# Kernel tuning notes

Hardware: AMD Instinct MI355X
Metric: run time of the kernel (lower is better)

Reference implementation:

```python
import jax, jax.numpy as jnp
import numpy as np

EMBED_DIM = 1024
NUM_HEADS = 16
HEAD_DIM = EMBED_DIM // NUM_HEADS


def setup_inputs() -> dict:
    key = jax.random.key(0)
    ks = jax.random.split(key, 11)
    B, S, D = 4, 2048, EMBED_DIM
    s = 1.0 / np.sqrt(D)
    return {
        "q": jax.random.normal(ks[0], (B, S, D), jnp.float32),
        "k": jax.random.normal(ks[1], (B, S, D), jnp.float32),
        "v": jax.random.normal(ks[2], (B, S, D), jnp.float32),
        "Wq": jax.random.normal(ks[3], (D, D), jnp.float32) * s,
        "bq": jnp.zeros((D,), jnp.float32),
        "Wk": jax.random.normal(ks[4], (D, D), jnp.float32) * s,
        "bk": jnp.zeros((D,), jnp.float32),
        "Wv": jax.random.normal(ks[5], (D, D), jnp.float32) * s,
        "bv": jnp.zeros((D,), jnp.float32),
        "Wo": jax.random.normal(ks[6], (D, D), jnp.float32) * s,
        "bo": jnp.zeros((D,), jnp.float32),
    }


def reference(q, k, v, Wq, bq, Wk, bk, Wv, bv, Wo, bo):
    B, S, D = q.shape
    H, Hd = NUM_HEADS, HEAD_DIM
    # projections, split heads -> [B, H, S, Hd]
    qh = (q @ Wq + bq).reshape(B, S, H, Hd).transpose(0, 2, 1, 3)
    kh = (k @ Wk + bk).reshape(B, S, H, Hd).transpose(0, 2, 1, 3)
    vh = (v @ Wv + bv).reshape(B, S, H, Hd).transpose(0, 2, 1, 3)
    scale = 1.0 / jnp.sqrt(jnp.asarray(Hd, qh.dtype))
    scores = jnp.einsum('bhqd,bhkd->bhqk', qh, kh) * scale  # [B,H,S,S]
    attn = jax.nn.softmax(scores, axis=-1)  # dropout = identity in eval
    out = jnp.einsum('bhqk,bhkd->bhqd', attn, vh)
    out = out.transpose(0, 2, 1, 3).reshape(B, S, D)
    return out @ Wo + bo
```

## Files before the change

### kernel.cpp

```cpp
#include <hip/hip_runtime.h>

typedef __attribute__((ext_vector_type(8))) __bf16 bf16x8;
typedef __attribute__((ext_vector_type(4))) __bf16 bf16x4;
typedef __attribute__((ext_vector_type(4))) float f32x4;
typedef __attribute__((ext_vector_type(16))) float f32x16;
typedef __attribute__((ext_vector_type(4))) unsigned int u32x4;

#define GLDS(g, l) __builtin_amdgcn_global_load_lds( \
    (const __attribute__((address_space(1))) void*)(g), \
    (__attribute__((address_space(3))) void*)(l), 16, 0, 0)

__device__ __forceinline__ unsigned cvtpk_bf16(float lo, float hi) {
    unsigned r;
    asm("v_cvt_pk_bf16_f32 %0, %1, %2" : "=v"(r) : "v"(lo), "v"(hi));
    return r;
}
__device__ __forceinline__ void pl32swap(unsigned& a, unsigned& b) {
    asm("v_permlane32_swap_b32 %0, %1" : "+v"(a), "+v"(b));
}

__global__ __launch_bounds__(256) void cvt_tile(const float* __restrict__ q,
                                                const float* __restrict__ k,
                                                const float* __restrict__ v,
                                                __bf16* __restrict__ qo,
                                                __bf16* __restrict__ ko,
                                                __bf16* __restrict__ vo) {
    const float* src = blockIdx.z == 0 ? q : blockIdx.z == 1 ? k : v;
    __bf16* dst = blockIdx.z == 0 ? qo : blockIdx.z == 1 ? ko : vo;
    __shared__ __align__(16) __bf16 sb[128 * 64];
    const int t = threadIdx.x;
    const int m0 = blockIdx.x * 128, kk0 = blockIdx.y * 64;
    #pragma unroll
    for (int i = 0; i < 4; i++) {
        int cid = i * 256 + t;
        int r = cid >> 3, cc = cid & 7;
        const float* p = src + (size_t)(m0 + r) * 1024 + kk0 + cc * 8;
        float4 a = *(const float4*)p;
        float4 b2 = *(const float4*)(p + 4);
        bf16x8 o;
        o[0] = (__bf16)a.x;  o[1] = (__bf16)a.y;  o[2] = (__bf16)a.z;  o[3] = (__bf16)a.w;
        o[4] = (__bf16)b2.x; o[5] = (__bf16)b2.y; o[6] = (__bf16)b2.z; o[7] = (__bf16)b2.w;
        *(bf16x8*)((char*)sb + r * 128 + ((cc ^ (r & 7)) << 4)) = o;
    }
    __syncthreads();
    #pragma unroll
    for (int i = 0; i < 4; i++) {
        int cid = i * 256 + t;
        int ch = cid >> 7, r = cid & 127;
        bf16x8 o = *(const bf16x8*)((const char*)sb + r * 128 + ((ch ^ (r & 7)) << 4));
        size_t off = (((size_t)blockIdx.x * 32 + blockIdx.y * 2 + (ch >> 2)) * 4 + (ch & 3)) * 1024
                   + (size_t)r * 8;
        *(bf16x8*)(dst + off) = o;
    }
}

__global__ __launch_bounds__(256) void wtrans2(const float* __restrict__ W0,
                                               const float* __restrict__ W1,
                                               const float* __restrict__ W2,
                                               const float* __restrict__ W3,
                                               __bf16* __restrict__ O0,
                                               __bf16* __restrict__ O1,
                                               __bf16* __restrict__ O2,
                                               __bf16* __restrict__ O3) {
    const int z = blockIdx.z;
    const float* W = z == 0 ? W0 : z == 1 ? W1 : z == 2 ? W2 : W3;
    __bf16* Wt2 = z == 0 ? O0 : z == 1 ? O1 : z == 2 ? O2 : O3;
    __shared__ float lw[64][65];
    const int kt = blockIdx.y * 64, nt = blockIdx.x * 64;
    const int t = threadIdx.x;
    const int r = t >> 4;
    const int c4 = (t & 15) * 4;
    #pragma unroll
    for (int rr = 0; rr < 64; rr += 16) {
        float4 vv = *(const float4*)&W[(size_t)(kt + r + rr) * 1024 + nt + c4];
        lw[r + rr][c4 + 0] = vv.x; lw[r + rr][c4 + 1] = vv.y;
        lw[r + rr][c4 + 2] = vv.z; lw[r + rr][c4 + 3] = vv.w;
    }
    __syncthreads();
    #pragma unroll
    for (int rr = 0; rr < 64; rr += 16) {
        int n = nt + r + rr;
        bf16x4 ov;
        #pragma unroll
        for (int i = 0; i < 4; i++) ov[i] = (__bf16)lw[c4 + i][r + rr];
        int kg = kt + c4;
        size_t off = (((size_t)(n >> 7) * 32 + (kg >> 5)) * 4 + ((kg & 31) >> 3)) * 1024
                   + (size_t)(n & 127) * 8 + (kg & 7);
        *(bf16x4*)&Wt2[off] = ov;
    }
}

__global__ __launch_bounds__(256, 2)
void gemm_tt(const __bf16* __restrict__ A0, const __bf16* __restrict__ A1,
             const __bf16* __restrict__ A2,
             const __bf16* __restrict__ B0, const __bf16* __restrict__ B1,
             const __bf16* __restrict__ B2,
             const float* __restrict__ bi0, const float* __restrict__ bi1,
             const float* __restrict__ bi2,
             void* __restrict__ C0, void* __restrict__ C1, void* __restrict__ C2,
             int mode0) {
    __shared__ __align__(16) __bf16 sA[3 * 4096];
    __shared__ __align__(16) __bf16 sB[3 * 4096];
    const int y = blockIdx.y;
    const __bf16* At  = y == 0 ? A0 : y == 1 ? A1 : A2;
    const __bf16* Bt2 = y == 0 ? B0 : y == 1 ? B1 : B2;
    const float* bias = y == 0 ? bi0 : y == 1 ? bi1 : bi2;
    void* Cout        = y == 0 ? C0 : y == 1 ? C1 : C2;
    const int mode    = y == 0 ? mode0 : y + 1;

    const int t = threadIdx.x, l = t & 63, w = t >> 6;
    const int wr = w >> 1, wc = w & 1;
    const int bid = blockIdx.x, slot = bid >> 3;
    const int ytile = (bid & 7) * 8 + (slot & 7);
    const int xtile = slot >> 3;
    const __bf16* Ab = At + (size_t)ytile * 131072;
    const __bf16* Bb = Bt2 + (size_t)xtile * 131072;

#define GISSUE(ks_, buf_) do { \
    GLDS(Ab + (ks_) * 4096 + t * 8,        (char*)sA + (buf_) * 8192 + t * 16); \
    GLDS(Ab + (ks_) * 4096 + 2048 + t * 8, (char*)sA + (buf_) * 8192 + 4096 + t * 16); \
    GLDS(Bb + (ks_) * 4096 + t * 8,        (char*)sB + (buf_) * 8192 + t * 16); \
    GLDS(Bb + (ks_) * 4096 + 2048 + t * 8, (char*)sB + (buf_) * 8192 + 4096 + t * 16); \
} while (0)

    f32x4 acc[4][4];
    #pragma unroll
    for (int i = 0; i < 4; i++)
        #pragma unroll
        for (int j = 0; j < 4; j++) acc[i][j] = (f32x4){0.f, 0.f, 0.f, 0.f};

    GISSUE(0, 0);
    GISSUE(1, 1);
    int cur = 0;
    #pragma unroll 1
    for (int ks = 0; ks < 32; ++ks) {
        if (ks < 31) asm volatile("s_waitcnt vmcnt(4)" ::: "memory");
        else         asm volatile("s_waitcnt vmcnt(0)" ::: "memory");
        __builtin_amdgcn_s_barrier();
        __builtin_amdgcn_sched_barrier(0);
        if (ks + 2 < 32) GISSUE(ks + 2, cur >= 1 ? cur - 1 : 2);
        const __bf16* bA = sA + cur * 4096;
        const __bf16* bB = sB + cur * 4096;
        bf16x8 af[4], bfr[4];
        #pragma unroll
        for (int i = 0; i < 4; i++)
            af[i] = *(const bf16x8*)(bA + (l >> 4) * 1024 + (wr * 64 + i * 16 + (l & 15)) * 8);
        #pragma unroll
        for (int j = 0; j < 4; j++)
            bfr[j] = *(const bf16x8*)(bB + (l >> 4) * 1024 + (wc * 64 + j * 16 + (l & 15)) * 8);
        __builtin_amdgcn_s_setprio(1);
        #pragma unroll
        for (int i = 0; i < 4; i++)
            #pragma unroll
            for (int j = 0; j < 4; j++)
                acc[i][j] = __builtin_amdgcn_mfma_f32_16x16x32_bf16(af[i], bfr[j], acc[i][j], 0, 0, 0);
        __builtin_amdgcn_s_setprio(0);
        cur = cur == 2 ? 0 : cur + 1;
    }
#undef GISSUE

    const int m0 = ytile * 128, n0 = xtile * 128;
    #pragma unroll
    for (int j = 0; j < 4; j++) {
        int col = n0 + wc * 64 + j * 16 + (l & 15);
        float bv = bias[col];
        #pragma unroll
        for (int i = 0; i < 4; i++) {
            #pragma unroll
            for (int r = 0; r < 4; r++) {
                int row = m0 + wr * 64 + i * 16 + (l >> 4) * 4 + r;
                float vvv = acc[i][j][r] + bv;
                if (mode == 0) {
                    ((float*)Cout)[(size_t)row * 1024 + col] = vvv;
                } else if (mode == 1) {
                    ((__bf16*)Cout)[(size_t)row * 1024 + col] = (__bf16)(vvv * 0.18033688f);
                } else if (mode == 2) {
                    int b_ = row >> 11, s_ = row & 2047, h_ = col >> 6, hd_ = col & 63;
                    size_t off = ((size_t)(b_ * 16 + h_) * 32 + (s_ >> 6)) * 4096
                               + (size_t)(hd_ >> 3) * 512 + (s_ & 63) * 8 + (hd_ & 7);
                    ((__bf16*)Cout)[off] = (__bf16)vvv;
                } else {
                    int b_ = row >> 11, s_ = row & 2047, h_ = col >> 6, d_ = col & 63;
                    size_t off = ((size_t)(b_ * 16 + h_) * 32 + (s_ >> 6)) * 4096
                               + (size_t)((s_ & 63) >> 3) * 512 + (size_t)d_ * 8 + (s_ & 7);
                    ((__bf16*)Cout)[off] = (__bf16)vvv;
                }
            }
        }
    }
}

__global__ __launch_bounds__(256, 2)
void attn_fwd(const __bf16* __restrict__ Qp, const __bf16* __restrict__ Kt,
              const __bf16* __restrict__ Vtt, __bf16* __restrict__ AOt) {
    constexpr int S = 2048, D = 1024;
    __shared__ __align__(16) __bf16 sK[3 * 4096];
    __shared__ __align__(16) __bf16 sV[3 * 4096];
    const int t = threadIdx.x, l = t & 63, w = t >> 6;
    const int c = l & 31, g = l >> 5;
    const int bid = blockIdx.x, slot = bid >> 3;
    const int bh = (slot >> 3) * 8 + (bid & 7);
    const int qb = slot & 7;
    const int b = bh >> 4, h = bh & 15;
    const int q0 = qb * 256;
    const __bf16* Kb = Kt + (size_t)bh * 131072;
    const __bf16* Vb = Vtt + (size_t)bh * 131072;

    bf16x8 qf[2][4];
    #pragma unroll
    for (int qh = 0; qh < 2; qh++) {
        const __bf16* qp = Qp + (size_t)(b * S + q0 + w * 64 + qh * 32 + c) * D + h * 64;
        #pragma unroll
        for (int ks = 0; ks < 4; ks++)
            qf[qh][ks] = *(const bf16x8*)(qp + ks * 16 + g * 8);
    }
    const __bf16 one = (__bf16)1.0f;
    const bf16x8 ones = {one, one, one, one, one, one, one, one};
    asm volatile("s_waitcnt vmcnt(0)" ::: "memory");

#define AISSUE(ti_, buf_) do { \
    GLDS(Kb + (ti_) * 4096 + t * 8,        (char*)sK + (buf_) * 8192 + t * 16); \
    GLDS(Kb + (ti_) * 4096 + 2048 + t * 8, (char*)sK + (buf_) * 8192 + 4096 + t * 16); \
    GLDS(Vb + (ti_) * 4096 + t * 8,        (char*)sV + (buf_) * 8192 + t * 16); \
    GLDS(Vb + (ti_) * 4096 + 2048 + t * 8, (char*)sV + (buf_) * 8192 + 4096 + t * 16); \
} while (0)

    f32x16 acc[2][2];
    acc[0][0] = (f32x16){}; acc[0][1] = (f32x16){};
    acc[1][0] = (f32x16){}; acc[1][1] = (f32x16){};
    f32x16 accl[2];
    accl[0] = (f32x16){}; accl[1] = (f32x16){};

    AISSUE(0, 0);
    AISSUE(1, 1);
    int cur = 0;
    #pragma unroll 1
    for (int tile = 0; tile < 32; ++tile) {
        if (tile < 31) asm volatile("s_waitcnt vmcnt(4)" ::: "memory");
        else           asm volatile("s_waitcnt vmcnt(0)" ::: "memory");
        __builtin_amdgcn_s_barrier();
        __builtin_amdgcn_sched_barrier(0);
        if (tile + 2 < 32) AISSUE(tile + 2, cur >= 1 ? cur - 1 : 2);
        const __bf16* bK = sK + cur * 4096;
        const __bf16* bV = sV + cur * 4096;
        #pragma unroll
        for (int kt = 0; kt < 2; kt++) {
            bf16x8 kf[4];
            #pragma unroll
            for (int ks = 0; ks < 4; ks++)
                kf[ks] = *(const bf16x8*)(bK + ((2 * ks + g) * 64 + kt * 32 + c) * 8);
            bf16x8 vq0[2], vq1[2];
            #pragma unroll
            for (int ti = 0; ti < 2; ti++) {
                vq0[ti] = *(const bf16x8*)(bV + ((4 * kt + g) * 64 + ti * 32 + c) * 8);
                vq1[ti] = *(const bf16x8*)(bV + ((4 * kt + 2 + g) * 64 + ti * 32 + c) * 8);
            }
            #pragma unroll
            for (int qh = 0; qh < 2; qh++) {
                f32x16 St = {};
                __builtin_amdgcn_s_setprio(1);
                St = __builtin_amdgcn_mfma_f32_32x32x16_bf16(kf[0], qf[qh][0], St, 0, 0, 0);
                St = __builtin_amdgcn_mfma_f32_32x32x16_bf16(kf[1], qf[qh][1], St, 0, 0, 0);
                St = __builtin_amdgcn_mfma_f32_32x32x16_bf16(kf[2], qf[qh][2], St, 0, 0, 0);
                St = __builtin_amdgcn_mfma_f32_32x32x16_bf16(kf[3], qf[qh][3], St, 0, 0, 0);
                __builtin_amdgcn_s_setprio(0);
                #pragma unroll
                for (int r2 = 0; r2 < 16; r2++)
                    St[r2] = __builtin_amdgcn_exp2f(St[r2]);
                unsigned w0 = cvtpk_bf16(St[0], St[1]),   w1 = cvtpk_bf16(St[2], St[3]);
                unsigned w2 = cvtpk_bf16(St[4], St[5]),   w3 = cvtpk_bf16(St[6], St[7]);
                unsigned w4 = cvtpk_bf16(St[8], St[9]),   w5 = cvtpk_bf16(St[10], St[11]);
                unsigned w6 = cvtpk_bf16(St[12], St[13]), w7 = cvtpk_bf16(St[14], St[15]);
                pl32swap(w0, w2); pl32swap(w1, w3);
                pl32swap(w4, w6); pl32swap(w5, w7);
                bf16x8 pa0 = __builtin_bit_cast(bf16x8, (u32x4){w0, w1, w2, w3});
                bf16x8 pa1 = __builtin_bit_cast(bf16x8, (u32x4){w4, w5, w6, w7});
                __builtin_amdgcn_s_setprio(1);
                acc[qh][0] = __builtin_amdgcn_mfma_f32_32x32x16_bf16(pa0, vq0[0], acc[qh][0], 0, 0, 0);
                acc[qh][1] = __builtin_amdgcn_mfma_f32_32x32x16_bf16(pa0, vq0[1], acc[qh][1], 0, 0, 0);
                acc[qh][0] = __builtin_amdgcn_mfma_f32_32x32x16_bf16(pa1, vq1[0], acc[qh][0], 0, 0, 0);
                acc[qh][1] = __builtin_amdgcn_mfma_f32_32x32x16_bf16(pa1, vq1[1], acc[qh][1], 0, 0, 0);
                accl[qh] = __builtin_amdgcn_mfma_f32_32x32x16_bf16(pa0, ones, accl[qh], 0, 0, 0);
                accl[qh] = __builtin_amdgcn_mfma_f32_32x32x16_bf16(pa1, ones, accl[qh], 0, 0, 0);
                __builtin_amdgcn_s_setprio(0);
            }
        }
        cur = cur == 2 ? 0 : cur + 1;
    }
#undef AISSUE

    #pragma unroll
    for (int qh = 0; qh < 2; qh++)
        #pragma unroll
        for (int rq = 0; rq < 4; rq++)
            #pragma unroll
            for (int rr2 = 0; rr2 < 4; rr2++) {
                int reg = rq * 4 + rr2;
                int rloc = rr2 + 8 * rq + 4 * g;
                float rn = __builtin_amdgcn_rcpf(accl[qh][reg]);
                int qloc = w * 64 + qh * 32 + rloc;
                int mt = b * 16 + qb * 2 + (qloc >> 7);
                int mr = qloc & 127;
                size_t base = ((size_t)mt * 32 + h * 2) * 4096 + (size_t)(c >> 3) * 1024
                            + (size_t)mr * 8 + (c & 7);
                AOt[base] = (__bf16)(acc[qh][0][reg] * rn);
                AOt[base + 4096] = (__bf16)(acc[qh][1][reg] * rn);
            }
}

extern "C" void kernel_launch(void* const* d_in, const int* in_sizes, int n_in,
                              void* d_out, int out_size, void* d_ws, size_t ws_size,
                              hipStream_t stream) {
    const float* q  = (const float*)d_in[0];
    const float* k  = (const float*)d_in[1];
    const float* v  = (const float*)d_in[2];
    const float* Wq = (const float*)d_in[3];
    const float* bq = (const float*)d_in[4];
    const float* Wk = (const float*)d_in[5];
    const float* bk = (const float*)d_in[6];
    const float* Wv = (const float*)d_in[7];
    const float* bv = (const float*)d_in[8];
    const float* Wo = (const float*)d_in[9];
    const float* bo = (const float*)d_in[10];

    char* ws = (char*)d_ws;
    const size_t MiB = 1024 * 1024;
    __bf16* Atq = (__bf16*)(ws);
    __bf16* Atk = (__bf16*)(ws + 16 * MiB);
    __bf16* Atv = (__bf16*)(ws + 32 * MiB);
    __bf16* W2q = (__bf16*)(ws + 48 * MiB);
    __bf16* W2k = (__bf16*)(ws + 50 * MiB);
    __bf16* W2v = (__bf16*)(ws + 52 * MiB);
    __bf16* W2o = (__bf16*)(ws + 54 * MiB);
    __bf16* Qp  = (__bf16*)(ws + 56 * MiB);
    __bf16* Kt  = (__bf16*)(ws + 72 * MiB);
    __bf16* Vtt = (__bf16*)(ws + 88 * MiB);
    __bf16* AOt = (__bf16*)(ws);

    cvt_tile<<<dim3(64, 16, 3), 256, 0, stream>>>(q, k, v, Atq, Atk, Atv);

    wtrans2<<<dim3(16, 16, 4), 256, 0, stream>>>(Wq, Wk, Wv, Wo, W2q, W2k, W2v, W2o);

    gemm_tt<<<dim3(512, 3), 256, 0, stream>>>(Atq, Atk, Atv, W2q, W2k, W2v,
                                              bq, bk, bv, Qp, Kt, Vtt, 1);

    attn_fwd<<<512, 256, 0, stream>>>(Qp, Kt, Vtt, AOt);

    gemm_tt<<<dim3(512, 1), 256, 0, stream>>>(AOt, AOt, AOt, W2o, W2o, W2o,
                                              bo, bo, bo, d_out, d_out, d_out, 0);
}
```

Baseline: 205.9 us.

## Deepen LDS pipeline to four stages and compute softmax row sums with VALU

Both the GEMM and attention kernels move from a 3-buffer to a 4-buffer LDS ring, prefetching three tiles ahead with adjusted vmcnt waits to hide more global latency. In attention, the softmax denominator is no longer computed with extra MFMAs against a ones vector; each lane sums its exp values, partial sums are combined with a cross-half shuffle, and reciprocals are shared through LDS. The GEMM is templated on QKV mode so the mode branch is resolved at compile time, and setprio hints in attention are removed. The larger LDS footprint (64 KB per block plus sL) may limit occupancy, and the row sums are now taken in fp32 before bf16 rounding.

```diff
diff --git a/kernel.cpp b/kernel.cpp
--- a/kernel.cpp
+++ b/kernel.cpp
@@ -84,12 +84,13 @@
         #pragma unroll
         for (int i = 0; i < 4; i++) ov[i] = (__bf16)lw[c4 + i][r + rr];
         int kg = kt + c4;
-        size_t off = (((size_t)(n >> 7) * 32 + (kg >> 5)) * 4 + ((kg & 31) >> 3)) * 1024
-                   + (size_t)(n & 127) * 8 + (kg & 7);
+        size_t off = (size_t)(n >> 7) * 131072 + (size_t)(kg >> 5) * 4096
+                   + (size_t)((kg >> 3) & 3) * 1024 + (size_t)(n & 127) * 8 + (kg & 7);
         *(bf16x4*)&Wt2[off] = ov;
     }
 }
 
+template <int QKV>
 __global__ __launch_bounds__(256, 2)
 void gemm_tt(const __bf16* __restrict__ A0, const __bf16* __restrict__ A1,
              const __bf16* __restrict__ A2,
@@ -97,16 +98,15 @@
              const __bf16* __restrict__ B2,
              const float* __restrict__ bi0, const float* __restrict__ bi1,
              const float* __restrict__ bi2,
-             void* __restrict__ C0, void* __restrict__ C1, void* __restrict__ C2,
-             int mode0) {
-    __shared__ __align__(16) __bf16 sA[3 * 4096];
-    __shared__ __align__(16) __bf16 sB[3 * 4096];
+             void* __restrict__ C0, void* __restrict__ C1, void* __restrict__ C2) {
+    __shared__ __align__(16) __bf16 sA[4 * 4096];
+    __shared__ __align__(16) __bf16 sB[4 * 4096];
     const int y = blockIdx.y;
-    const __bf16* At  = y == 0 ? A0 : y == 1 ? A1 : A2;
-    const __bf16* Bt2 = y == 0 ? B0 : y == 1 ? B1 : B2;
-    const float* bias = y == 0 ? bi0 : y == 1 ? bi1 : bi2;
-    void* Cout        = y == 0 ? C0 : y == 1 ? C1 : C2;
-    const int mode    = y == 0 ? mode0 : y + 1;
+    const __bf16* At  = QKV ? (y == 0 ? A0 : y == 1 ? A1 : A2) : A0;
+    const __bf16* Bt2 = QKV ? (y == 0 ? B0 : y == 1 ? B1 : B2) : B0;
+    const float* bias = QKV ? (y == 0 ? bi0 : y == 1 ? bi1 : bi2) : bi0;
+    void* Cout        = QKV ? (y == 0 ? C0 : y == 1 ? C1 : C2) : C0;
+    const int mode    = QKV ? y + 1 : 0;
 
     const int t = threadIdx.x, l = t & 63, w = t >> 6;
     const int wr = w >> 1, wc = w & 1;
@@ -131,14 +131,16 @@
 
     GISSUE(0, 0);
     GISSUE(1, 1);
+    GISSUE(2, 2);
     int cur = 0;
     #pragma unroll 1
     for (int ks = 0; ks < 32; ++ks) {
-        if (ks < 31) asm volatile("s_waitcnt vmcnt(4)" ::: "memory");
-        else         asm volatile("s_waitcnt vmcnt(0)" ::: "memory");
+        if (ks < 30)      asm volatile("s_waitcnt vmcnt(8)" ::: "memory");
+        else if (ks == 30) asm volatile("s_waitcnt vmcnt(4)" ::: "memory");
+        else               asm volatile("s_waitcnt vmcnt(0)" ::: "memory");
         __builtin_amdgcn_s_barrier();
         __builtin_amdgcn_sched_barrier(0);
-        if (ks + 2 < 32) GISSUE(ks + 2, cur >= 1 ? cur - 1 : 2);
+        if (ks + 3 < 32) GISSUE(ks + 3, (cur + 3) & 3);
         const __bf16* bA = sA + cur * 4096;
         const __bf16* bB = sB + cur * 4096;
         bf16x8 af[4], bfr[4];
@@ -155,7 +157,7 @@
             for (int j = 0; j < 4; j++)
                 acc[i][j] = __builtin_amdgcn_mfma_f32_16x16x32_bf16(af[i], bfr[j], acc[i][j], 0, 0, 0);
         __builtin_amdgcn_s_setprio(0);
-        cur = cur == 2 ? 0 : cur + 1;
+        cur = (cur + 1) & 3;
     }
 #undef GISSUE
 
@@ -194,8 +196,9 @@
 void attn_fwd(const __bf16* __restrict__ Qp, const __bf16* __restrict__ Kt,
               const __bf16* __restrict__ Vtt, __bf16* __restrict__ AOt) {
     constexpr int S = 2048, D = 1024;
-    __shared__ __align__(16) __bf16 sK[3 * 4096];
-    __shared__ __align__(16) __bf16 sV[3 * 4096];
+    __shared__ __align__(16) __bf16 sK[4 * 4096];
+    __shared__ __align__(16) __bf16 sV[4 * 4096];
+    __shared__ float sL[4][64];
     const int t = threadIdx.x, l = t & 63, w = t >> 6;
     const int c = l & 31, g = l >> 5;
     const int bid = blockIdx.x, slot = bid >> 3;
@@ -214,8 +217,6 @@
         for (int ks = 0; ks < 4; ks++)
             qf[qh][ks] = *(const bf16x8*)(qp + ks * 16 + g * 8);
     }
-    const __bf16 one = (__bf16)1.0f;
-    const bf16x8 ones = {one, one, one, one, one, one, one, one};
     asm volatile("s_waitcnt vmcnt(0)" ::: "memory");
 
 #define AISSUE(ti_, buf_) do { \
@@ -228,19 +229,20 @@
     f32x16 acc[2][2];
     acc[0][0] = (f32x16){}; acc[0][1] = (f32x16){};
     acc[1][0] = (f32x16){}; acc[1][1] = (f32x16){};
-    f32x16 accl[2];
-    accl[0] = (f32x16){}; accl[1] = (f32x16){};
+    float ls[2] = {0.f, 0.f};
 
     AISSUE(0, 0);
     AISSUE(1, 1);
+    AISSUE(2, 2);
     int cur = 0;
     #pragma unroll 1
     for (int tile = 0; tile < 32; ++tile) {
-        if (tile < 31) asm volatile("s_waitcnt vmcnt(4)" ::: "memory");
-        else           asm volatile("s_waitcnt vmcnt(0)" ::: "memory");
+        if (tile < 30)       asm volatile("s_waitcnt vmcnt(8)" ::: "memory");
+        else if (tile == 30) asm volatile("s_waitcnt vmcnt(4)" ::: "memory");
+        else                 asm volatile("s_waitcnt vmcnt(0)" ::: "memory");
         __builtin_amdgcn_s_barrier();
         __builtin_amdgcn_sched_barrier(0);
-        if (tile + 2 < 32) AISSUE(tile + 2, cur >= 1 ? cur - 1 : 2);
+        if (tile + 3 < 32) AISSUE(tile + 3, (cur + 3) & 3);
         const __bf16* bK = sK + cur * 4096;
         const __bf16* bV = sV + cur * 4096;
         #pragma unroll
@@ -258,15 +260,16 @@
             #pragma unroll
             for (int qh = 0; qh < 2; qh++) {
                 f32x16 St = {};
-                __builtin_amdgcn_s_setprio(1);
                 St = __builtin_amdgcn_mfma_f32_32x32x16_bf16(kf[0], qf[qh][0], St, 0, 0, 0);
                 St = __builtin_amdgcn_mfma_f32_32x32x16_bf16(kf[1], qf[qh][1], St, 0, 0, 0);
                 St = __builtin_amdgcn_mfma_f32_32x32x16_bf16(kf[2], qf[qh][2], St, 0, 0, 0);
                 St = __builtin_amdgcn_mfma_f32_32x32x16_bf16(kf[3], qf[qh][3], St, 0, 0, 0);
-                __builtin_amdgcn_s_setprio(0);
                 #pragma unroll
-                for (int r2 = 0; r2 < 16; r2++)
-                    St[r2] = __builtin_amdgcn_exp2f(St[r2]);
+                for (int r2 = 0; r2 < 16; r2++) {
+                    float p = __builtin_amdgcn_exp2f(St[r2]);
+                    ls[qh] += p;
+                    St[r2] = p;
+                }
                 unsigned w0 = cvtpk_bf16(St[0], St[1]),   w1 = cvtpk_bf16(St[2], St[3]);
                 unsigned w2 = cvtpk_bf16(St[4], St[5]),   w3 = cvtpk_bf16(St[6], St[7]);
                 unsigned w4 = cvtpk_bf16(St[8], St[9]),   w5 = cvtpk_bf16(St[10], St[11]);
@@ -275,19 +278,20 @@
                 pl32swap(w4, w6); pl32swap(w5, w7);
                 bf16x8 pa0 = __builtin_bit_cast(bf16x8, (u32x4){w0, w1, w2, w3});
                 bf16x8 pa1 = __builtin_bit_cast(bf16x8, (u32x4){w4, w5, w6, w7});
-                __builtin_amdgcn_s_setprio(1);
                 acc[qh][0] = __builtin_amdgcn_mfma_f32_32x32x16_bf16(pa0, vq0[0], acc[qh][0], 0, 0, 0);
                 acc[qh][1] = __builtin_amdgcn_mfma_f32_32x32x16_bf16(pa0, vq0[1], acc[qh][1], 0, 0, 0);
                 acc[qh][0] = __builtin_amdgcn_mfma_f32_32x32x16_bf16(pa1, vq1[0], acc[qh][0], 0, 0, 0);
                 acc[qh][1] = __builtin_amdgcn_mfma_f32_32x32x16_bf16(pa1, vq1[1], acc[qh][1], 0, 0, 0);
-                accl[qh] = __builtin_amdgcn_mfma_f32_32x32x16_bf16(pa0, ones, accl[qh], 0, 0, 0);
-                accl[qh] = __builtin_amdgcn_mfma_f32_32x32x16_bf16(pa1, ones, accl[qh], 0, 0, 0);
-                __builtin_amdgcn_s_setprio(0);
             }
         }
-        cur = cur == 2 ? 0 : cur + 1;
+        cur = (cur + 1) & 3;
     }
 #undef AISSUE
+
+    float tt0 = ls[0] + __shfl_xor(ls[0], 32);
+    float tt1 = ls[1] + __shfl_xor(ls[1], 32);
+    if (l < 32) { sL[w][l] = 1.0f / tt0; sL[w][32 + l] = 1.0f / tt1; }
+    __syncthreads();
 
     #pragma unroll
     for (int qh = 0; qh < 2; qh++)
@@ -297,7 +301,7 @@
             for (int rr2 = 0; rr2 < 4; rr2++) {
                 int reg = rq * 4 + rr2;
                 int rloc = rr2 + 8 * rq + 4 * g;
-                float rn = __builtin_amdgcn_rcpf(accl[qh][reg]);
+                float rn = sL[w][qh * 32 + rloc];
                 int qloc = w * 64 + qh * 32 + rloc;
                 int mt = b * 16 + qb * 2 + (qloc >> 7);
                 int mr = qloc & 127;
@@ -341,11 +345,11 @@
 
     wtrans2<<<dim3(16, 16, 4), 256, 0, stream>>>(Wq, Wk, Wv, Wo, W2q, W2k, W2v, W2o);
 
-    gemm_tt<<<dim3(512, 3), 256, 0, stream>>>(Atq, Atk, Atv, W2q, W2k, W2v,
-                                              bq, bk, bv, Qp, Kt, Vtt, 1);
+    gemm_tt<1><<<dim3(512, 3), 256, 0, stream>>>(Atq, Atk, Atv, W2q, W2k, W2v,
+                                                 bq, bk, bv, Qp, Kt, Vtt);
 
     attn_fwd<<<512, 256, 0, stream>>>(Qp, Kt, Vtt, AOt);
 
-    gemm_tt<<<dim3(512, 1), 256, 0, stream>>>(AOt, AOt, AOt, W2o, W2o, W2o,
-                                              bo, bo, bo, d_out, d_out, d_out, 0);
-}
+    gemm_tt<0><<<dim3(512, 1), 256, 0, stream>>>(AOt, AOt, AOt, W2o, W2o, W2o,
+                                                 bo, bo, bo, d_out, d_out, d_out);
+}
```

After: 217.3 us. +5.5%, slower.

## Fuse fp32-to-bf16 input conversion into QKV GEMM and compute softmax row sums with VALU

Applied to the files above, without the earlier changes.

Removes the separate cvt_tile kernel. The QKV projection GEMM now reads fp32 activations directly, converts them in registers and writes bf16 tiles into a double-buffered LDS, which cuts a full 48 MiB write and read round trip. In attention, the row-sum MFMAs against a ones vector are replaced by VALU accumulation of exp values plus a cross-lane shuffle and an LDS reduction. The next-tile prefetch is also moved after the compute, and the setprio hints are dropped. The output GEMM is specialised into a simpler fp32-output kernel, and the QKV kernel now asks for 3 blocks per SM through its launch bounds.

```diff
diff --git a/kernel.cpp b/kernel.cpp
--- a/kernel.cpp
+++ b/kernel.cpp
@@ -17,41 +17,6 @@
 }
 __device__ __forceinline__ void pl32swap(unsigned& a, unsigned& b) {
     asm("v_permlane32_swap_b32 %0, %1" : "+v"(a), "+v"(b));
-}
-
-__global__ __launch_bounds__(256) void cvt_tile(const float* __restrict__ q,
-                                                const float* __restrict__ k,
-                                                const float* __restrict__ v,
-                                                __bf16* __restrict__ qo,
-                                                __bf16* __restrict__ ko,
-                                                __bf16* __restrict__ vo) {
-    const float* src = blockIdx.z == 0 ? q : blockIdx.z == 1 ? k : v;
-    __bf16* dst = blockIdx.z == 0 ? qo : blockIdx.z == 1 ? ko : vo;
-    __shared__ __align__(16) __bf16 sb[128 * 64];
-    const int t = threadIdx.x;
-    const int m0 = blockIdx.x * 128, kk0 = blockIdx.y * 64;
-    #pragma unroll
-    for (int i = 0; i < 4; i++) {
-        int cid = i * 256 + t;
-        int r = cid >> 3, cc = cid & 7;
-        const float* p = src + (size_t)(m0 + r) * 1024 + kk0 + cc * 8;
-        float4 a = *(const float4*)p;
-        float4 b2 = *(const float4*)(p + 4);
-        bf16x8 o;
-        o[0] = (__bf16)a.x;  o[1] = (__bf16)a.y;  o[2] = (__bf16)a.z;  o[3] = (__bf16)a.w;
-        o[4] = (__bf16)b2.x; o[5] = (__bf16)b2.y; o[6] = (__bf16)b2.z; o[7] = (__bf16)b2.w;
-        *(bf16x8*)((char*)sb + r * 128 + ((cc ^ (r & 7)) << 4)) = o;
-    }
-    __syncthreads();
-    #pragma unroll
-    for (int i = 0; i < 4; i++) {
-        int cid = i * 256 + t;
-        int ch = cid >> 7, r = cid & 127;
-        bf16x8 o = *(const bf16x8*)((const char*)sb + r * 128 + ((ch ^ (r & 7)) << 4));
-        size_t off = (((size_t)blockIdx.x * 32 + blockIdx.y * 2 + (ch >> 2)) * 4 + (ch & 3)) * 1024
-                   + (size_t)r * 8;
-        *(bf16x8*)(dst + off) = o;
-    }
 }
 
 __global__ __launch_bounds__(256) void wtrans2(const float* __restrict__ W0,
@@ -84,30 +49,133 @@
         #pragma unroll
         for (int i = 0; i < 4; i++) ov[i] = (__bf16)lw[c4 + i][r + rr];
         int kg = kt + c4;
-        size_t off = (((size_t)(n >> 7) * 32 + (kg >> 5)) * 4 + ((kg & 31) >> 3)) * 1024
-                   + (size_t)(n & 127) * 8 + (kg & 7);
+        size_t off = (size_t)(n >> 7) * 131072 + (size_t)(kg >> 5) * 4096
+                   + (size_t)((kg >> 3) & 3) * 1024 + (size_t)(n & 127) * 8 + (kg & 7);
         *(bf16x4*)&Wt2[off] = ov;
     }
 }
 
-__global__ __launch_bounds__(256, 2)
-void gemm_tt(const __bf16* __restrict__ A0, const __bf16* __restrict__ A1,
-             const __bf16* __restrict__ A2,
-             const __bf16* __restrict__ B0, const __bf16* __restrict__ B1,
-             const __bf16* __restrict__ B2,
-             const float* __restrict__ bi0, const float* __restrict__ bi1,
-             const float* __restrict__ bi2,
-             void* __restrict__ C0, void* __restrict__ C1, void* __restrict__ C2,
-             int mode0) {
-    __shared__ __align__(16) __bf16 sA[3 * 4096];
+__global__ __launch_bounds__(256, 3)
+void gemm_f32a(const float* __restrict__ A0, const float* __restrict__ A1,
+               const float* __restrict__ A2,
+               const __bf16* __restrict__ B0, const __bf16* __restrict__ B1,
+               const __bf16* __restrict__ B2,
+               const float* __restrict__ bi0, const float* __restrict__ bi1,
+               const float* __restrict__ bi2,
+               void* __restrict__ C0, void* __restrict__ C1, void* __restrict__ C2) {
+    __shared__ __align__(16) __bf16 sA[2 * 4096];
     __shared__ __align__(16) __bf16 sB[3 * 4096];
     const int y = blockIdx.y;
-    const __bf16* At  = y == 0 ? A0 : y == 1 ? A1 : A2;
+    const float* A    = y == 0 ? A0 : y == 1 ? A1 : A2;
     const __bf16* Bt2 = y == 0 ? B0 : y == 1 ? B1 : B2;
     const float* bias = y == 0 ? bi0 : y == 1 ? bi1 : bi2;
     void* Cout        = y == 0 ? C0 : y == 1 ? C1 : C2;
-    const int mode    = y == 0 ? mode0 : y + 1;
-
+    const int mode    = y + 1;
+
+    const int t = threadIdx.x, l = t & 63, w = t >> 6;
+    const int wr = w >> 1, wc = w & 1;
+    const int bid = blockIdx.x, slot = bid >> 3;
+    const int ytile = (bid & 7) * 8 + (slot & 7);
+    const int xtile = slot >> 3;
+    const float* Ag = A + (size_t)(ytile * 128 + (t & 127)) * 1024 + (t >> 7) * 16;
+    const __bf16* Bb = Bt2 + (size_t)xtile * 131072;
+    char* const aw = (char*)sA + ((t >> 7) * 2) * 2048 + (t & 127) * 16;
+
+    float4 rA0, rA1, rA2, rA3;
+#define LOADA(T_) do { \
+    const float* p_ = Ag + (T_) * 32; \
+    rA0 = *(const float4*)p_;        rA1 = *(const float4*)(p_ + 4); \
+    rA2 = *(const float4*)(p_ + 8);  rA3 = *(const float4*)(p_ + 12); \
+} while (0)
+#define WRITEA(buf_) do { \
+    bf16x8 o0_, o1_; \
+    o0_[0] = (__bf16)rA0.x; o0_[1] = (__bf16)rA0.y; o0_[2] = (__bf16)rA0.z; o0_[3] = (__bf16)rA0.w; \
+    o0_[4] = (__bf16)rA1.x; o0_[5] = (__bf16)rA1.y; o0_[6] = (__bf16)rA1.z; o0_[7] = (__bf16)rA1.w; \
+    o1_[0] = (__bf16)rA2.x; o1_[1] = (__bf16)rA2.y; o1_[2] = (__bf16)rA2.z; o1_[3] = (__bf16)rA2.w; \
+    o1_[4] = (__bf16)rA3.x; o1_[5] = (__bf16)rA3.y; o1_[6] = (__bf16)rA3.z; o1_[7] = (__bf16)rA3.w; \
+    *(bf16x8*)(aw + (buf_) * 8192) = o0_; \
+    *(bf16x8*)(aw + (buf_) * 8192 + 2048) = o1_; \
+} while (0)
+#define GLDSB(T_, buf_) do { \
+    GLDS(Bb + (T_) * 4096 + t * 8,        (char*)sB + (buf_) * 8192 + t * 16); \
+    GLDS(Bb + (T_) * 4096 + 2048 + t * 8, (char*)sB + (buf_) * 8192 + 4096 + t * 16); \
+} while (0)
+
+    f32x4 acc[4][4];
+    #pragma unroll
+    for (int i = 0; i < 4; i++)
+        #pragma unroll
+        for (int j = 0; j < 4; j++) acc[i][j] = (f32x4){0.f, 0.f, 0.f, 0.f};
+
+    LOADA(0); GLDSB(0, 0);
+    WRITEA(0);
+    LOADA(1); GLDSB(1, 1);
+
+    int bcur = 0;
+    #pragma unroll 1
+    for (int T = 0; T < 32; ++T) {
+        if (T <= 30) asm volatile("s_waitcnt vmcnt(6) lgkmcnt(0)" ::: "memory");
+        else         asm volatile("s_waitcnt vmcnt(0) lgkmcnt(0)" ::: "memory");
+        __builtin_amdgcn_s_barrier();
+        __builtin_amdgcn_sched_barrier(0);
+        if (T <= 30) WRITEA((T + 1) & 1);
+        if (T <= 29) { LOADA(T + 2); GLDSB(T + 2, bcur >= 1 ? bcur - 1 : 2); }
+        const char* bA = (const char*)sA + (T & 1) * 8192;
+        const char* bB = (const char*)sB + bcur * 8192;
+        bf16x8 af[4], bfr[4];
+        #pragma unroll
+        for (int i = 0; i < 4; i++)
+            af[i] = *(const bf16x8*)(bA + (l >> 4) * 2048 + (wr * 64 + i * 16 + (l & 15)) * 16);
+        #pragma unroll
+        for (int j = 0; j < 4; j++)
+            bfr[j] = *(const bf16x8*)(bB + (l >> 4) * 2048 + (wc * 64 + j * 16 + (l & 15)) * 16);
+        __builtin_amdgcn_s_setprio(1);
+        #pragma unroll
+        for (int i = 0; i < 4; i++)
+            #pragma unroll
+            for (int j = 0; j < 4; j++)
+                acc[i][j] = __builtin_amdgcn_mfma_f32_16x16x32_bf16(af[i], bfr[j], acc[i][j], 0, 0, 0);
+        __builtin_amdgcn_s_setprio(0);
+        bcur = bcur == 2 ? 0 : bcur + 1;
+    }
+#undef LOADA
+#undef WRITEA
+#undef GLDSB
+
+    const int m0 = ytile * 128, n0 = xtile * 128;
+    #pragma unroll
+    for (int j = 0; j < 4; j++) {
+        int col = n0 + wc * 64 + j * 16 + (l & 15);
+        float bv = bias[col];
+        #pragma unroll
+        for (int i = 0; i < 4; i++) {
+            #pragma unroll
+            for (int r = 0; r < 4; r++) {
+                int row = m0 + wr * 64 + i * 16 + (l >> 4) * 4 + r;
+                float vvv = acc[i][j][r] + bv;
+                if (mode == 1) {
+                    ((__bf16*)Cout)[(size_t)row * 1024 + col] = (__bf16)(vvv * 0.18033688f);
+                } else if (mode == 2) {
+                    int b_ = row >> 11, s_ = row & 2047, h_ = col >> 6, hd_ = col & 63;
+                    size_t off = ((size_t)(b_ * 16 + h_) * 32 + (s_ >> 6)) * 4096
+                               + (size_t)(hd_ >> 3) * 512 + (s_ & 63) * 8 + (hd_ & 7);
+                    ((__bf16*)Cout)[off] = (__bf16)vvv;
+                } else {
+                    int b_ = row >> 11, s_ = row & 2047, h_ = col >> 6, d_ = col & 63;
+                    size_t off = ((size_t)(b_ * 16 + h_) * 32 + (s_ >> 6)) * 4096
+                               + (size_t)((s_ & 63) >> 3) * 512 + (size_t)d_ * 8 + (s_ & 7);
+                    ((__bf16*)Cout)[off] = (__bf16)vvv;
+                }
+            }
+        }
+    }
+}
+
+__global__ __launch_bounds__(256, 2)
+void gemm_tt(const __bf16* __restrict__ At, const __bf16* __restrict__ Bt2,
+             const float* __restrict__ bias, float* __restrict__ Cout) {
+    __shared__ __align__(16) __bf16 sA[3 * 4096];
+    __shared__ __align__(16) __bf16 sB[3 * 4096];
     const int t = threadIdx.x, l = t & 63, w = t >> 6;
     const int wr = w >> 1, wc = w & 1;
     const int bid = blockIdx.x, slot = bid >> 3;
@@ -169,22 +237,7 @@
             #pragma unroll
             for (int r = 0; r < 4; r++) {
                 int row = m0 + wr * 64 + i * 16 + (l >> 4) * 4 + r;
-                float vvv = acc[i][j][r] + bv;
-                if (mode == 0) {
-                    ((float*)Cout)[(size_t)row * 1024 + col] = vvv;
-                } else if (mode == 1) {
-                    ((__bf16*)Cout)[(size_t)row * 1024 + col] = (__bf16)(vvv * 0.18033688f);
-                } else if (mode == 2) {
-                    int b_ = row >> 11, s_ = row & 2047, h_ = col >> 6, hd_ = col & 63;
-                    size_t off = ((size_t)(b_ * 16 + h_) * 32 + (s_ >> 6)) * 4096
-                               + (size_t)(hd_ >> 3) * 512 + (s_ & 63) * 8 + (hd_ & 7);
-                    ((__bf16*)Cout)[off] = (__bf16)vvv;
-                } else {
-                    int b_ = row >> 11, s_ = row & 2047, h_ = col >> 6, d_ = col & 63;
-                    size_t off = ((size_t)(b_ * 16 + h_) * 32 + (s_ >> 6)) * 4096
-                               + (size_t)((s_ & 63) >> 3) * 512 + (size_t)d_ * 8 + (s_ & 7);
-                    ((__bf16*)Cout)[off] = (__bf16)vvv;
-                }
+                Cout[(size_t)row * 1024 + col] = acc[i][j][r] + bv;
             }
         }
     }
@@ -196,6 +249,7 @@
     constexpr int S = 2048, D = 1024;
     __shared__ __align__(16) __bf16 sK[3 * 4096];
     __shared__ __align__(16) __bf16 sV[3 * 4096];
+    __shared__ float sL[4][64];
     const int t = threadIdx.x, l = t & 63, w = t >> 6;
     const int c = l & 31, g = l >> 5;
     const int bid = blockIdx.x, slot = bid >> 3;
@@ -214,8 +268,6 @@
         for (int ks = 0; ks < 4; ks++)
             qf[qh][ks] = *(const bf16x8*)(qp + ks * 16 + g * 8);
     }
-    const __bf16 one = (__bf16)1.0f;
-    const bf16x8 ones = {one, one, one, one, one, one, one, one};
     asm volatile("s_waitcnt vmcnt(0)" ::: "memory");
 
 #define AISSUE(ti_, buf_) do { \
@@ -228,8 +280,7 @@
     f32x16 acc[2][2];
     acc[0][0] = (f32x16){}; acc[0][1] = (f32x16){};
     acc[1][0] = (f32x16){}; acc[1][1] = (f32x16){};
-    f32x16 accl[2];
-    accl[0] = (f32x16){}; accl[1] = (f32x16){};
+    float ls[2] = {0.f, 0.f};
 
     AISSUE(0, 0);
     AISSUE(1, 1);
@@ -240,7 +291,6 @@
         else           asm volatile("s_waitcnt vmcnt(0)" ::: "memory");
         __builtin_amdgcn_s_barrier();
         __builtin_amdgcn_sched_barrier(0);
-        if (tile + 2 < 32) AISSUE(tile + 2, cur >= 1 ? cur - 1 : 2);
         const __bf16* bK = sK + cur * 4096;
         const __bf16* bV = sV + cur * 4096;
         #pragma unroll
@@ -258,15 +308,16 @@
             #pragma unroll
             for (int qh = 0; qh < 2; qh++) {
                 f32x16 St = {};
-                __builtin_amdgcn_s_setprio(1);
                 St = __builtin_amdgcn_mfma_f32_32x32x16_bf16(kf[0], qf[qh][0], St, 0, 0, 0);
                 St = __builtin_amdgcn_mfma_f32_32x32x16_bf16(kf[1], qf[qh][1], St, 0, 0, 0);
                 St = __builtin_amdgcn_mfma_f32_32x32x16_bf16(kf[2], qf[qh][2], St, 0, 0, 0);
                 St = __builtin_amdgcn_mfma_f32_32x32x16_bf16(kf[3], qf[qh][3], St, 0, 0, 0);
-                __builtin_amdgcn_s_setprio(0);
                 #pragma unroll
-                for (int r2 = 0; r2 < 16; r2++)
-                    St[r2] = __builtin_amdgcn_exp2f(St[r2]);
+                for (int r2 = 0; r2 < 16; r2++) {
+                    float p = __builtin_amdgcn_exp2f(St[r2]);
+                    ls[qh] += p;
+                    St[r2] = p;
+                }
                 unsigned w0 = cvtpk_bf16(St[0], St[1]),   w1 = cvtpk_bf16(St[2], St[3]);
                 unsigned w2 = cvtpk_bf16(St[4], St[5]),   w3 = cvtpk_bf16(St[6], St[7]);
                 unsigned w4 = cvtpk_bf16(St[8], St[9]),   w5 = cvtpk_bf16(St[10], St[11]);
@@ -275,19 +326,21 @@
                 pl32swap(w4, w6); pl32swap(w5, w7);
                 bf16x8 pa0 = __builtin_bit_cast(bf16x8, (u32x4){w0, w1, w2, w3});
                 bf16x8 pa1 = __builtin_bit_cast(bf16x8, (u32x4){w4, w5, w6, w7});
-                __builtin_amdgcn_s_setprio(1);
                 acc[qh][0] = __builtin_amdgcn_mfma_f32_32x32x16_bf16(pa0, vq0[0], acc[qh][0], 0, 0, 0);
                 acc[qh][1] = __builtin_amdgcn_mfma_f32_32x32x16_bf16(pa0, vq0[1], acc[qh][1], 0, 0, 0);
                 acc[qh][0] = __builtin_amdgcn_mfma_f32_32x32x16_bf16(pa1, vq1[0], acc[qh][0], 0, 0, 0);
                 acc[qh][1] = __builtin_amdgcn_mfma_f32_32x32x16_bf16(pa1, vq1[1], acc[qh][1], 0, 0, 0);
-                accl[qh] = __builtin_amdgcn_mfma_f32_32x32x16_bf16(pa0, ones, accl[qh], 0, 0, 0);
-                accl[qh] = __builtin_amdgcn_mfma_f32_32x32x16_bf16(pa1, ones, accl[qh], 0, 0, 0);
-                __builtin_amdgcn_s_setprio(0);
             }
         }
+        if (tile + 2 < 32) AISSUE(tile + 2, cur >= 1 ? cur - 1 : 2);
         cur = cur == 2 ? 0 : cur + 1;
     }
 #undef AISSUE
+
+    float tt0 = ls[0] + __shfl_xor(ls[0], 32);
+    float tt1 = ls[1] + __shfl_xor(ls[1], 32);
+    if (l < 32) { sL[w][l] = 1.0f / tt0; sL[w][32 + l] = 1.0f / tt1; }
+    __syncthreads();
 
     #pragma unroll
     for (int qh = 0; qh < 2; qh++)
@@ -297,7 +350,7 @@
             for (int rr2 = 0; rr2 < 4; rr2++) {
                 int reg = rq * 4 + rr2;
                 int rloc = rr2 + 8 * rq + 4 * g;
-                float rn = __builtin_amdgcn_rcpf(accl[qh][reg]);
+                float rn = sL[w][qh * 32 + rloc];
                 int qloc = w * 64 + qh * 32 + rloc;
                 int mt = b * 16 + qb * 2 + (qloc >> 7);
                 int mr = qloc & 127;
@@ -325,9 +378,7 @@
 
     char* ws = (char*)d_ws;
     const size_t MiB = 1024 * 1024;
-    __bf16* Atq = (__bf16*)(ws);
-    __bf16* Atk = (__bf16*)(ws + 16 * MiB);
-    __bf16* Atv = (__bf16*)(ws + 32 * MiB);
+    __bf16* AOt = (__bf16*)(ws);
     __bf16* W2q = (__bf16*)(ws + 48 * MiB);
     __bf16* W2k = (__bf16*)(ws + 50 * MiB);
     __bf16* W2v = (__bf16*)(ws + 52 * MiB);
@@ -335,17 +386,13 @@
     __bf16* Qp  = (__bf16*)(ws + 56 * MiB);
     __bf16* Kt  = (__bf16*)(ws + 72 * MiB);
     __bf16* Vtt = (__bf16*)(ws + 88 * MiB);
-    __bf16* AOt = (__bf16*)(ws);
-
-    cvt_tile<<<dim3(64, 16, 3), 256, 0, stream>>>(q, k, v, Atq, Atk, Atv);
 
     wtrans2<<<dim3(16, 16, 4), 256, 0, stream>>>(Wq, Wk, Wv, Wo, W2q, W2k, W2v, W2o);
 
-    gemm_tt<<<dim3(512, 3), 256, 0, stream>>>(Atq, Atk, Atv, W2q, W2k, W2v,
-                                              bq, bk, bv, Qp, Kt, Vtt, 1);
+    gemm_f32a<<<dim3(512, 3), 256, 0, stream>>>(q, k, v, W2q, W2k, W2v,
+                                                bq, bk, bv, Qp, Kt, Vtt);
 
     attn_fwd<<<512, 256, 0, stream>>>(Qp, Kt, Vtt, AOt);
 
-    gemm_tt<<<dim3(512, 1), 256, 0, stream>>>(AOt, AOt, AOt, W2o, W2o, W2o,
-                                              bo, bo, bo, d_out, d_out, d_out, 0);
-}
+    gemm_tt<<<512, 256, 0, stream>>>(AOt, W2o, bo, (float*)d_out);
+}
```

Result: slower. 234.5 us (+13.9%).
